# Optimization experiments

Hardware: AMD Instinct MI355X
Metric: run time of the kernel (lower is better)

The kernel has to match this reference:

```python
import math
import jax, jax.numpy as jnp
import numpy as np

N, D, E, H = 4096, 512, 64, 8
LN_EPS = 1e-5


def setup_inputs() -> dict:
    key = jax.random.key(0)
    ks = jax.random.split(key, 6)
    return {
        "x": jax.random.normal(ks[0], (N, D), jnp.float32),
        "wq": jax.random.normal(ks[1], (H, D, E), jnp.float32) * 0.05,
        "wk": jax.random.normal(ks[2], (H, D, E), jnp.float32) * 0.05,
        "wv": jax.random.normal(ks[3], (H, D, E), jnp.float32) * 0.05,
        "w_mh": jax.random.normal(ks[4], (H * E, D), jnp.float32) * 0.05,
        "ln1_g": jnp.ones((D,), jnp.float32),
        "ln1_b": jnp.zeros((D,), jnp.float32),
        "ffn_w": jax.random.normal(ks[5], (D, D), jnp.float32) * 0.05,  # torch Linear weight [out,in]
        "ffn_b": jnp.zeros((D,), jnp.float32),
        "ln2_g": jnp.ones((D,), jnp.float32),
        "ln2_b": jnp.zeros((D,), jnp.float32),
    }


def _layernorm(y, g, b):
    m = y.mean(-1, keepdims=True)
    v = ((y - m) ** 2).mean(-1, keepdims=True)
    return (y - m) * jax.lax.rsqrt(v + LN_EPS) * g + b


def reference(x, wq, wk, wv, w_mh, ln1_g, ln1_b, ffn_w, ffn_b, ln2_g, ln2_b):
    dk = math.sqrt(wk.shape[-1])  # sqrt(embedding_size), as in the torch code
    q = jnp.einsum('nd,hde->hne', x, wq)  # [H,N,E]
    k = jnp.einsum('nd,hde->hne', x, wk)
    v = jnp.einsum('nd,hde->hne', x, wv)
    scores = jax.nn.softmax(jnp.einsum('hne,hme->hnm', q, k) / dk, axis=-1)  # [H,N,N]
    z = jnp.einsum('hnm,hme->hne', scores, v)  # [H,N,E]
    concat_z = jnp.transpose(z, (1, 0, 2)).reshape(x.shape[0], -1)  # [N, H*E]
    transformed_z = concat_z @ w_mh  # [N, D]
    normed_z = _layernorm(transformed_z + x, ln1_g, ln1_b)
    out = normed_z @ ffn_w.T + ffn_b  # nn.Linear
    return _layernorm(out + normed_z, ln2_g, ln2_b)
```

## Files before the change

kernel.cpp:

```cpp
#include <hip/hip_runtime.h>

#define NN 4096
#define DD 512
#define EE 64
#define HH 8

typedef _Float16 f16;
typedef f16 f16x4 __attribute__((ext_vector_type(4)));
typedef f16 f16x8 __attribute__((ext_vector_type(8)));
typedef float f32x4 __attribute__((ext_vector_type(4)));

__global__ __launch_bounds__(256) void cvt_kernel(const float* __restrict__ s, f16* __restrict__ d, int n)
{
    int i = (blockIdx.x * 256 + threadIdx.x) * 4;
    if (i < n) {
        float4 t = *(const float4*)(s + i);
        f16x4 h = { (f16)t.x, (f16)t.y, (f16)t.z, (f16)t.w };
        *(f16x4*)(d + i) = h;
    }
}

__global__ __launch_bounds__(256) void transpose_cvt_kernel(
    const float* __restrict__ src, f16* __restrict__ dst, int R, int C)
{
    __shared__ float t[32][33];
    const int z = blockIdx.z;
    src += (size_t)z * R * C;
    dst += (size_t)z * R * C;
    const int bx = blockIdx.x * 32;
    const int by = blockIdx.y * 32;
    const int tx = threadIdx.x & 31;
    const int ty = threadIdx.x >> 5;
    #pragma unroll
    for (int i = 0; i < 4; ++i) {
        int r = ty + i * 8;
        t[r][tx] = src[(size_t)(by + r) * C + bx + tx];
    }
    __syncthreads();
    #pragma unroll
    for (int i = 0; i < 4; ++i) {
        int c = ty + i * 8;
        dst[(size_t)(bx + c) * R + by + tx] = (f16)t[tx][c];
    }
}

__global__ __launch_bounds__(256) void qkv_mfma_kernel(
    const f16* __restrict__ A, const f16* __restrict__ BT,
    f16* __restrict__ qh, f16* __restrict__ kh, f16* __restrict__ vTh)
{
    __shared__ f16 As[64][72];
    __shared__ f16 Bs[64][72];
    const int tid = threadIdx.x;
    const int n0 = blockIdx.x * 64;
    const int cb = blockIdx.y;
    const int sel = cb >> 3, h = cb & 7;
    const f16* Arow = A + (size_t)n0 * DD;
    const f16* Brow = BT + (size_t)cb * 64 * DD;

    const int lane = tid & 63, wave = tid >> 6;
    const int l16 = lane & 15, quad = lane >> 4;
    const int m0 = wave * 16;

    f32x4 acc[4];
    #pragma unroll
    for (int t = 0; t < 4; ++t) acc[t] = (f32x4){0.f, 0.f, 0.f, 0.f};

    for (int kt = 0; kt < DD; kt += 64) {
        __syncthreads();
        #pragma unroll
        for (int i = 0; i < 2; ++i) {
            int idx = tid + i * 256;
            int r = idx >> 3, c8 = (idx & 7) * 8;
            *(f16x8*)(&As[r][c8]) = *(const f16x8*)(Arow + (size_t)r * DD + kt + c8);
            *(f16x8*)(&Bs[r][c8]) = *(const f16x8*)(Brow + (size_t)r * DD + kt + c8);
        }
        __syncthreads();
        #pragma unroll
        for (int kk = 0; kk < 64; kk += 32) {
            f16x8 a = *(const f16x8*)(&As[m0 + l16][kk + quad * 8]);
            #pragma unroll
            for (int t = 0; t < 4; ++t) {
                f16x8 b = *(const f16x8*)(&Bs[t * 16 + l16][kk + quad * 8]);
                acc[t] = __builtin_amdgcn_mfma_f32_16x16x32_f16(a, b, acc[t], 0, 0, 0);
            }
        }
    }

    if (sel == 2) {
        #pragma unroll
        for (int t = 0; t < 4; ++t) {
            int e = t * 16 + l16;
            #pragma unroll
            for (int r = 0; r < 4; ++r)
                vTh[((size_t)h * EE + e) * NN + n0 + m0 + quad * 4 + r] = (f16)acc[t][r];
        }
    } else {
        f16* o = (sel == 0) ? qh : kh;
        const float s = (sel == 0) ? 0.125f : 1.0f;
        #pragma unroll
        for (int r = 0; r < 4; ++r) {
            int row = n0 + m0 + quad * 4 + r;
            #pragma unroll
            for (int t = 0; t < 4; ++t)
                o[(size_t)h * NN * EE + (size_t)row * EE + t * 16 + l16] = (f16)(acc[t][r] * s);
        }
    }
}

#define BQ 64
#define BK 64
#define SPLITS 2
#define LQ (EE + 8)
#define LV (BK + 12)

__global__ __launch_bounds__(256) void attn_mfma_kernel(
    const f16* __restrict__ q, const f16* __restrict__ k,
    const f16* __restrict__ vT, float* __restrict__ Opart, float* __restrict__ lpart)
{
    __shared__ f16 Qs[BQ][LQ];
    __shared__ f16 Ks[BK][LQ];
    __shared__ f16 VsT[EE][LV];
    __shared__ f16 Ps[BQ][LV];

    const int tid = threadIdx.x;
    const int h = blockIdx.y;
    const int n0 = blockIdx.x * BQ;
    const int sp = blockIdx.z;
    const int wave = tid >> 6;
    const int lane = tid & 63;
    const int l16 = lane & 15;
    const int quad = lane >> 4;
    const int m0 = wave * 16;

    const f16* qh = q + (size_t)h * NN * EE;
    const f16* kh = k + (size_t)h * NN * EE;
    const f16* vh = vT + (size_t)h * NN * EE;

    #pragma unroll
    for (int i = 0; i < 2; ++i) {
        int idx = tid + i * 256;
        int row = idx >> 3, c8 = (idx & 7) * 8;
        *(f16x8*)(&Qs[row][c8]) = *(const f16x8*)(qh + (size_t)(n0 + row) * EE + c8);
    }
    __syncthreads();

    f16x8 qf0 = *(const f16x8*)(&Qs[m0 + l16][quad * 8]);
    f16x8 qf1 = *(const f16x8*)(&Qs[m0 + l16][32 + quad * 8]);

    float lp[4] = {0.f, 0.f, 0.f, 0.f};
    f32x4 O[4];
    #pragma unroll
    for (int t = 0; t < 4; ++t) O[t] = (f32x4){0.f, 0.f, 0.f, 0.f};

    const int k_begin = sp * (NN / SPLITS);
    const int k_end = k_begin + (NN / SPLITS);

    const int srow = tid >> 3, sc8 = (tid & 7) * 8;
    const int srow2 = (tid + 256) >> 3, sc82 = ((tid + 256) & 7) * 8;

    f16x8 kr0 = *(const f16x8*)(kh + (size_t)(k_begin + srow) * EE + sc8);
    f16x8 kr1 = *(const f16x8*)(kh + (size_t)(k_begin + srow2) * EE + sc82);
    f16x8 vr0 = *(const f16x8*)(vh + (size_t)srow * NN + k_begin + sc8);
    f16x8 vr1 = *(const f16x8*)(vh + (size_t)srow2 * NN + k_begin + sc82);

    for (int kt = k_begin; kt < k_end; kt += BK) {
        __syncthreads();
        *(f16x8*)(&Ks[srow][sc8]) = kr0;
        *(f16x8*)(&Ks[srow2][sc82]) = kr1;
        *(f16x8*)(&VsT[srow][sc8]) = vr0;
        *(f16x8*)(&VsT[srow2][sc82]) = vr1;
        __syncthreads();

        if (kt + BK < k_end) {
            kr0 = *(const f16x8*)(kh + (size_t)(kt + BK + srow) * EE + sc8);
            kr1 = *(const f16x8*)(kh + (size_t)(kt + BK + srow2) * EE + sc82);
            vr0 = *(const f16x8*)(vh + (size_t)srow * NN + kt + BK + sc8);
            vr1 = *(const f16x8*)(vh + (size_t)srow2 * NN + kt + BK + sc82);
        }

        f32x4 S[4];
        #pragma unroll
        for (int t = 0; t < 4; ++t) {
            f16x8 b0 = *(const f16x8*)(&Ks[t * 16 + l16][quad * 8]);
            f16x8 b1 = *(const f16x8*)(&Ks[t * 16 + l16][32 + quad * 8]);
            f32x4 s = {0.f, 0.f, 0.f, 0.f};
            s = __builtin_amdgcn_mfma_f32_16x16x32_f16(qf0, b0, s, 0, 0, 0);
            s = __builtin_amdgcn_mfma_f32_16x16x32_f16(qf1, b1, s, 0, 0, 0);
            S[t] = s;
        }

        #pragma unroll
        for (int r = 0; r < 4; ++r) {
            float p0 = __expf(S[0][r]);
            float p1 = __expf(S[1][r]);
            float p2 = __expf(S[2][r]);
            float p3 = __expf(S[3][r]);
            lp[r] += (p0 + p1) + (p2 + p3);
            const int prow = m0 + quad * 4 + r;
            Ps[prow][0 * 16 + l16] = (f16)p0;
            Ps[prow][1 * 16 + l16] = (f16)p1;
            Ps[prow][2 * 16 + l16] = (f16)p2;
            Ps[prow][3 * 16 + l16] = (f16)p3;
        }

        f16x8 a0 = *(const f16x8*)(&Ps[m0 + l16][quad * 8]);
        f16x8 a1 = *(const f16x8*)(&Ps[m0 + l16][32 + quad * 8]);
        #pragma unroll
        for (int t = 0; t < 4; ++t) {
            f16x8 b0 = *(const f16x8*)(&VsT[t * 16 + l16][quad * 8]);
            f16x8 b1 = *(const f16x8*)(&VsT[t * 16 + l16][32 + quad * 8]);
            O[t] = __builtin_amdgcn_mfma_f32_16x16x32_f16(a0, b0, O[t], 0, 0, 0);
            O[t] = __builtin_amdgcn_mfma_f32_16x16x32_f16(a1, b1, O[t], 0, 0, 0);
        }
    }

    #pragma unroll
    for (int r = 0; r < 4; ++r) {
        float s = lp[r];
        s += __shfl_xor(s, 1);
        s += __shfl_xor(s, 2);
        s += __shfl_xor(s, 4);
        s += __shfl_xor(s, 8);
        const int row = n0 + m0 + quad * 4 + r;
        if (l16 == 0)
            lpart[(size_t)sp * HH * NN + (size_t)h * NN + row] = s;
        #pragma unroll
        for (int t = 0; t < 4; ++t)
            Opart[(size_t)sp * NN * DD + (size_t)row * DD + h * EE + t * 16 + l16] = O[t][r];
    }
}

__global__ __launch_bounds__(256) void attn_combine_kernel(
    const float* __restrict__ Opart, const float* __restrict__ lpart, f16* __restrict__ zh)
{
    const size_t idx = ((size_t)blockIdx.x * 256 + threadIdx.x) * 8;
    const int n = (int)(idx >> 9);
    const int c = (int)(idx & 511);
    const int h = c >> 6;
    const float l = lpart[(size_t)h * NN + n] + lpart[(size_t)HH * NN + (size_t)h * NN + n];
    const float inv = 1.f / l;
    f32x4 a0 = *(const f32x4*)(Opart + idx);
    f32x4 a1 = *(const f32x4*)(Opart + idx + 4);
    f32x4 b0 = *(const f32x4*)(Opart + (size_t)NN * DD + idx);
    f32x4 b1 = *(const f32x4*)(Opart + (size_t)NN * DD + idx + 4);
    f16x8 o;
    #pragma unroll
    for (int i = 0; i < 4; ++i) {
        o[i]     = (f16)((a0[i] + b0[i]) * inv);
        o[i + 4] = (f16)((a1[i] + b1[i]) * inv);
    }
    *(f16x8*)(zh + idx) = o;
}

__global__ __launch_bounds__(256) void gemm_mfma_kernel(
    const f16* __restrict__ A, const f16* __restrict__ BT,
    const float* __restrict__ bias, const float* __restrict__ resid32,
    const f16* __restrict__ resid16, float* __restrict__ out)
{
    __shared__ f16 As[64][72];
    __shared__ f16 Bs[64][72];
    const int tid = threadIdx.x;
    const int n0 = blockIdx.x * 64;
    const int j0 = blockIdx.y * 64;
    const f16* Arow = A + (size_t)n0 * DD;
    const f16* Brow = BT + (size_t)j0 * DD;

    const int lane = tid & 63, wave = tid >> 6;
    const int l16 = lane & 15, quad = lane >> 4;
    const int m0 = wave * 16;

    f32x4 acc[4];
    #pragma unroll
    for (int t = 0; t < 4; ++t) acc[t] = (f32x4){0.f, 0.f, 0.f, 0.f};

    for (int kt = 0; kt < DD; kt += 64) {
        __syncthreads();
        #pragma unroll
        for (int i = 0; i < 2; ++i) {
            int idx = tid + i * 256;
            int r = idx >> 3, c8 = (idx & 7) * 8;
            *(f16x8*)(&As[r][c8]) = *(const f16x8*)(Arow + (size_t)r * DD + kt + c8);
            *(f16x8*)(&Bs[r][c8]) = *(const f16x8*)(Brow + (size_t)r * DD + kt + c8);
        }
        __syncthreads();
        #pragma unroll
        for (int kk = 0; kk < 64; kk += 32) {
            f16x8 a = *(const f16x8*)(&As[m0 + l16][kk + quad * 8]);
            #pragma unroll
            for (int t = 0; t < 4; ++t) {
                f16x8 b = *(const f16x8*)(&Bs[t * 16 + l16][kk + quad * 8]);
                acc[t] = __builtin_amdgcn_mfma_f32_16x16x32_f16(a, b, acc[t], 0, 0, 0);
            }
        }
    }

    #pragma unroll
    for (int r = 0; r < 4; ++r) {
        int row = n0 + m0 + quad * 4 + r;
        #pragma unroll
        for (int t = 0; t < 4; ++t) {
            int col = j0 + t * 16 + l16;
            float v = acc[t][r];
            if (bias)    v += bias[col];
            if (resid32) v += resid32[(size_t)row * DD + col];
            if (resid16) v += (float)resid16[(size_t)row * DD + col];
            out[(size_t)row * DD + col] = v;
        }
    }
}

__global__ __launch_bounds__(256) void ln_kernel(
    const float* __restrict__ y, const float* __restrict__ g, const float* __restrict__ b,
    f16* __restrict__ oh, float* __restrict__ of)
{
    const int lane = threadIdx.x & 63, wave = threadIdx.x >> 6;
    const int row = blockIdx.x * 4 + wave;
    const float* yr = y + (size_t)row * DD;
    f32x4 v0 = *(const f32x4*)(yr + lane * 4);
    f32x4 v1 = *(const f32x4*)(yr + 256 + lane * 4);
    float s = (v0[0] + v0[1]) + (v0[2] + v0[3]) + (v1[0] + v1[1]) + (v1[2] + v1[3]);
    float q = (v0[0]*v0[0] + v0[1]*v0[1]) + (v0[2]*v0[2] + v0[3]*v0[3])
            + (v1[0]*v1[0] + v1[1]*v1[1]) + (v1[2]*v1[2] + v1[3]*v1[3]);
    #pragma unroll
    for (int o = 1; o < 64; o <<= 1) { s += __shfl_xor(s, o); q += __shfl_xor(q, o); }
    float mean = s * (1.f / DD);
    float var = q * (1.f / DD) - mean * mean;
    float inv = rsqrtf(var + 1e-5f);

    f32x4 g0 = *(const f32x4*)(g + lane * 4);
    f32x4 g1 = *(const f32x4*)(g + 256 + lane * 4);
    f32x4 b0 = *(const f32x4*)(b + lane * 4);
    f32x4 b1 = *(const f32x4*)(b + 256 + lane * 4);
    f32x4 o0, o1;
    #pragma unroll
    for (int i = 0; i < 4; ++i) {
        o0[i] = (v0[i] - mean) * inv * g0[i] + b0[i];
        o1[i] = (v1[i] - mean) * inv * g1[i] + b1[i];
    }
    if (oh) {
        f16x4 h0 = { (f16)o0[0], (f16)o0[1], (f16)o0[2], (f16)o0[3] };
        f16x4 h1 = { (f16)o1[0], (f16)o1[1], (f16)o1[2], (f16)o1[3] };
        *(f16x4*)(oh + (size_t)row * DD + lane * 4) = h0;
        *(f16x4*)(oh + (size_t)row * DD + 256 + lane * 4) = h1;
    }
    if (of) {
        *(f32x4*)(of + (size_t)row * DD + lane * 4) = o0;
        *(f32x4*)(of + (size_t)row * DD + 256 + lane * 4) = o1;
    }
}

extern "C" void kernel_launch(void* const* d_in, const int* in_sizes, int n_in,
                              void* d_out, int out_size, void* d_ws, size_t ws_size,
                              hipStream_t stream) {
    const float* x     = (const float*)d_in[0];
    const float* wq    = (const float*)d_in[1];
    const float* wk    = (const float*)d_in[2];
    const float* wv    = (const float*)d_in[3];
    const float* w_mh  = (const float*)d_in[4];
    const float* ln1_g = (const float*)d_in[5];
    const float* ln1_b = (const float*)d_in[6];
    const float* ffn_w = (const float*)d_in[7];
    const float* ffn_b = (const float*)d_in[8];
    const float* ln2_g = (const float*)d_in[9];
    const float* ln2_b = (const float*)d_in[10];
    float* out = (float*)d_out;

    char* base = (char*)d_ws;
    float* Opart = (float*)base;
    float* lpart = Opart + (size_t)2 * NN * DD;
    f16* xh   = (f16*)base;
    float* y  = (float*)base;
    f16* p = (f16*)(base + ((size_t)2 * NN * DD + (size_t)2 * HH * NN) * sizeof(float));
    f16* wqkvT  = p; p += (size_t)3 * HH * EE * DD;
    f16* wmhT   = p; p += (size_t)DD * DD;
    f16* ffnT   = p; p += (size_t)DD * DD;
    f16* qh     = p; p += (size_t)HH * NN * EE;
    f16* kh     = p; p += (size_t)HH * NN * EE;
    f16* vTh    = p; p += (size_t)HH * NN * EE;
    f16* zh     = p; p += (size_t)NN * DD;
    f16* nzh    = p; p += (size_t)NN * DD;

    cvt_kernel<<<dim3(NN * DD / 1024), 256, 0, stream>>>(x, xh, NN * DD);
    cvt_kernel<<<dim3(DD * DD / 1024), 256, 0, stream>>>(ffn_w, ffnT, DD * DD);
    transpose_cvt_kernel<<<dim3(EE / 32, DD / 32, HH), 256, 0, stream>>>(wq, wqkvT, DD, EE);
    transpose_cvt_kernel<<<dim3(EE / 32, DD / 32, HH), 256, 0, stream>>>(wk, wqkvT + (size_t)HH * EE * DD, DD, EE);
    transpose_cvt_kernel<<<dim3(EE / 32, DD / 32, HH), 256, 0, stream>>>(wv, wqkvT + (size_t)2 * HH * EE * DD, DD, EE);
    transpose_cvt_kernel<<<dim3(DD / 32, DD / 32, 1), 256, 0, stream>>>(w_mh, wmhT, DD, DD);

    qkv_mfma_kernel<<<dim3(NN / 64, 24), 256, 0, stream>>>(xh, wqkvT, qh, kh, vTh);
    attn_mfma_kernel<<<dim3(NN / BQ, HH, SPLITS), 256, 0, stream>>>(qh, kh, vTh, Opart, lpart);
    attn_combine_kernel<<<dim3(NN * DD / 2048), 256, 0, stream>>>(Opart, lpart, zh);
    gemm_mfma_kernel<<<dim3(NN / 64, DD / 64), 256, 0, stream>>>(zh, wmhT, nullptr, x, nullptr, y);
    ln_kernel<<<dim3(NN / 4), 256, 0, stream>>>(y, ln1_g, ln1_b, nzh, nullptr);
    gemm_mfma_kernel<<<dim3(NN / 64, DD / 64), 256, 0, stream>>>(nzh, ffnT, ffn_b, nullptr, nzh, y);
    ln_kernel<<<dim3(NN / 4), 256, 0, stream>>>(y, ln2_g, ln2_b, nullptr, out);
}
```

Before: 217.1 us.

## Compute transposed attention scores so P stays in registers, use exp2, adaptive splits

```diff
diff --git a/kernel.cpp b/kernel.cpp
--- a/kernel.cpp
+++ b/kernel.cpp
@@ -9,6 +9,8 @@
 typedef f16 f16x4 __attribute__((ext_vector_type(4)));
 typedef f16 f16x8 __attribute__((ext_vector_type(8)));
 typedef float f32x4 __attribute__((ext_vector_type(4)));
+
+__device__ __forceinline__ float hexp2(float x) { return __builtin_amdgcn_exp2f(x); }
 
 __global__ __launch_bounds__(256) void cvt_kernel(const float* __restrict__ s, f16* __restrict__ d, int n)
 {
@@ -96,7 +98,7 @@
         }
     } else {
         f16* o = (sel == 0) ? qh : kh;
-        const float s = (sel == 0) ? 0.125f : 1.0f;
+        const float s = (sel == 0) ? 0.125f * 1.44269504088896f : 1.0f;
         #pragma unroll
         for (int r = 0; r < 4; ++r) {
             int row = n0 + m0 + quad * 4 + r;
@@ -109,23 +111,20 @@
 
 #define BQ 64
 #define BK 64
-#define SPLITS 2
-#define LQ (EE + 8)
-#define LV (BK + 12)
+#define LK (BK + 12)
 
 __global__ __launch_bounds__(256) void attn_mfma_kernel(
     const f16* __restrict__ q, const f16* __restrict__ k,
     const f16* __restrict__ vT, float* __restrict__ Opart, float* __restrict__ lpart)
 {
-    __shared__ f16 Qs[BQ][LQ];
-    __shared__ f16 Ks[BK][LQ];
-    __shared__ f16 VsT[EE][LV];
-    __shared__ f16 Ps[BQ][LV];
+    __shared__ f16 Ks[BK][LK];
+    __shared__ f16 VsT[EE][LK];
 
     const int tid = threadIdx.x;
     const int h = blockIdx.y;
     const int n0 = blockIdx.x * BQ;
     const int sp = blockIdx.z;
+    const int nsp = gridDim.z;
     const int wave = tid >> 6;
     const int lane = tid & 63;
     const int l16 = lane & 15;
@@ -136,27 +135,22 @@
     const f16* kh = k + (size_t)h * NN * EE;
     const f16* vh = vT + (size_t)h * NN * EE;
 
-    #pragma unroll
-    for (int i = 0; i < 2; ++i) {
-        int idx = tid + i * 256;
-        int row = idx >> 3, c8 = (idx & 7) * 8;
-        *(f16x8*)(&Qs[row][c8]) = *(const f16x8*)(qh + (size_t)(n0 + row) * EE + c8);
-    }
-    __syncthreads();
-
-    f16x8 qf0 = *(const f16x8*)(&Qs[m0 + l16][quad * 8]);
-    f16x8 qf1 = *(const f16x8*)(&Qs[m0 + l16][32 + quad * 8]);
-
-    float lp[4] = {0.f, 0.f, 0.f, 0.f};
+    f16x8 qf0 = *(const f16x8*)(qh + (size_t)(n0 + m0 + l16) * EE + quad * 8);
+    f16x8 qf1 = *(const f16x8*)(qh + (size_t)(n0 + m0 + l16) * EE + 32 + quad * 8);
+
+    float lp = 0.f;
     f32x4 O[4];
     #pragma unroll
     for (int t = 0; t < 4; ++t) O[t] = (f32x4){0.f, 0.f, 0.f, 0.f};
 
-    const int k_begin = sp * (NN / SPLITS);
-    const int k_end = k_begin + (NN / SPLITS);
+    const int span = NN / nsp;
+    const int k_begin = sp * span;
+    const int k_end = k_begin + span;
 
     const int srow = tid >> 3, sc8 = (tid & 7) * 8;
     const int srow2 = (tid + 256) >> 3, sc82 = ((tid + 256) & 7) * 8;
+    #define KPERM(kk_) (((kk_) & 0x23) | (((kk_) & 0x04) << 2) | (((kk_) & 0x18) >> 1))
+    const int prow1 = KPERM(srow), prow2 = KPERM(srow2);
 
     f16x8 kr0 = *(const f16x8*)(kh + (size_t)(k_begin + srow) * EE + sc8);
     f16x8 kr1 = *(const f16x8*)(kh + (size_t)(k_begin + srow2) * EE + sc82);
@@ -165,8 +159,8 @@
 
     for (int kt = k_begin; kt < k_end; kt += BK) {
         __syncthreads();
-        *(f16x8*)(&Ks[srow][sc8]) = kr0;
-        *(f16x8*)(&Ks[srow2][sc82]) = kr1;
+        *(f16x8*)(&Ks[prow1][sc8]) = kr0;
+        *(f16x8*)(&Ks[prow2][sc82]) = kr1;
         *(f16x8*)(&VsT[srow][sc8]) = vr0;
         *(f16x8*)(&VsT[srow2][sc82]) = vr1;
         __syncthreads();
@@ -178,76 +172,69 @@
             vr1 = *(const f16x8*)(vh + (size_t)srow2 * NN + kt + BK + sc82);
         }
 
-        f32x4 S[4];
+        f32x4 st[4];
         #pragma unroll
         for (int t = 0; t < 4; ++t) {
-            f16x8 b0 = *(const f16x8*)(&Ks[t * 16 + l16][quad * 8]);
-            f16x8 b1 = *(const f16x8*)(&Ks[t * 16 + l16][32 + quad * 8]);
+            f16x8 a0 = *(const f16x8*)(&Ks[t * 16 + l16][quad * 8]);
+            f16x8 a1 = *(const f16x8*)(&Ks[t * 16 + l16][32 + quad * 8]);
             f32x4 s = {0.f, 0.f, 0.f, 0.f};
-            s = __builtin_amdgcn_mfma_f32_16x16x32_f16(qf0, b0, s, 0, 0, 0);
-            s = __builtin_amdgcn_mfma_f32_16x16x32_f16(qf1, b1, s, 0, 0, 0);
-            S[t] = s;
-        }
-
-        #pragma unroll
-        for (int r = 0; r < 4; ++r) {
-            float p0 = __expf(S[0][r]);
-            float p1 = __expf(S[1][r]);
-            float p2 = __expf(S[2][r]);
-            float p3 = __expf(S[3][r]);
-            lp[r] += (p0 + p1) + (p2 + p3);
-            const int prow = m0 + quad * 4 + r;
-            Ps[prow][0 * 16 + l16] = (f16)p0;
-            Ps[prow][1 * 16 + l16] = (f16)p1;
-            Ps[prow][2 * 16 + l16] = (f16)p2;
-            Ps[prow][3 * 16 + l16] = (f16)p3;
-        }
-
-        f16x8 a0 = *(const f16x8*)(&Ps[m0 + l16][quad * 8]);
-        f16x8 a1 = *(const f16x8*)(&Ps[m0 + l16][32 + quad * 8]);
+            s = __builtin_amdgcn_mfma_f32_16x16x32_f16(a0, qf0, s, 0, 0, 0);
+            s = __builtin_amdgcn_mfma_f32_16x16x32_f16(a1, qf1, s, 0, 0, 0);
+            st[t] = s;
+        }
+
+        f16x8 bf[2];
         #pragma unroll
         for (int t = 0; t < 4; ++t) {
-            f16x8 b0 = *(const f16x8*)(&VsT[t * 16 + l16][quad * 8]);
-            f16x8 b1 = *(const f16x8*)(&VsT[t * 16 + l16][32 + quad * 8]);
-            O[t] = __builtin_amdgcn_mfma_f32_16x16x32_f16(a0, b0, O[t], 0, 0, 0);
-            O[t] = __builtin_amdgcn_mfma_f32_16x16x32_f16(a1, b1, O[t], 0, 0, 0);
-        }
-    }
-
-    #pragma unroll
-    for (int r = 0; r < 4; ++r) {
-        float s = lp[r];
-        s += __shfl_xor(s, 1);
-        s += __shfl_xor(s, 2);
-        s += __shfl_xor(s, 4);
-        s += __shfl_xor(s, 8);
-        const int row = n0 + m0 + quad * 4 + r;
-        if (l16 == 0)
-            lpart[(size_t)sp * HH * NN + (size_t)h * NN + row] = s;
-        #pragma unroll
-        for (int t = 0; t < 4; ++t)
-            Opart[(size_t)sp * NN * DD + (size_t)row * DD + h * EE + t * 16 + l16] = O[t][r];
-    }
+            float p0 = hexp2(st[t][0]);
+            float p1 = hexp2(st[t][1]);
+            float p2 = hexp2(st[t][2]);
+            float p3 = hexp2(st[t][3]);
+            lp += (p0 + p1) + (p2 + p3);
+            f16x8& b = bf[t >> 1];
+            const int o = (t & 1) * 4;
+            b[o + 0] = (f16)p0; b[o + 1] = (f16)p1;
+            b[o + 2] = (f16)p2; b[o + 3] = (f16)p3;
+        }
+
+        #pragma unroll
+        for (int te = 0; te < 4; ++te) {
+            f16x8 v0 = *(const f16x8*)(&VsT[te * 16 + l16][quad * 8]);
+            f16x8 v1 = *(const f16x8*)(&VsT[te * 16 + l16][32 + quad * 8]);
+            O[te] = __builtin_amdgcn_mfma_f32_16x16x32_f16(v0, bf[0], O[te], 0, 0, 0);
+            O[te] = __builtin_amdgcn_mfma_f32_16x16x32_f16(v1, bf[1], O[te], 0, 0, 0);
+        }
+    }
+
+    const int row = n0 + m0 + l16;
+    lp += __shfl_xor(lp, 16);
+    lp += __shfl_xor(lp, 32);
+    if (quad == 0)
+        lpart[(size_t)sp * HH * NN + (size_t)h * NN + row] = lp;
+    #pragma unroll
+    for (int te = 0; te < 4; ++te)
+        *(f32x4*)(Opart + ((size_t)sp * NN + row) * DD + h * EE + te * 16 + quad * 4) = O[te];
 }
 
 __global__ __launch_bounds__(256) void attn_combine_kernel(
-    const float* __restrict__ Opart, const float* __restrict__ lpart, f16* __restrict__ zh)
+    const float* __restrict__ Opart, const float* __restrict__ lpart, f16* __restrict__ zh, int nsp)
 {
     const size_t idx = ((size_t)blockIdx.x * 256 + threadIdx.x) * 8;
     const int n = (int)(idx >> 9);
-    const int c = (int)(idx & 511);
-    const int h = c >> 6;
-    const float l = lpart[(size_t)h * NN + n] + lpart[(size_t)HH * NN + (size_t)h * NN + n];
+    const int h = (int)((idx & 511) >> 6);
+    float l = 0.f;
+    for (int s = 0; s < nsp; ++s) l += lpart[(size_t)s * HH * NN + (size_t)h * NN + n];
     const float inv = 1.f / l;
-    f32x4 a0 = *(const f32x4*)(Opart + idx);
-    f32x4 a1 = *(const f32x4*)(Opart + idx + 4);
-    f32x4 b0 = *(const f32x4*)(Opart + (size_t)NN * DD + idx);
-    f32x4 b1 = *(const f32x4*)(Opart + (size_t)NN * DD + idx + 4);
+    f32x4 a0 = {0.f,0.f,0.f,0.f}, a1 = {0.f,0.f,0.f,0.f};
+    for (int s = 0; s < nsp; ++s) {
+        a0 += *(const f32x4*)(Opart + (size_t)s * NN * DD + idx);
+        a1 += *(const f32x4*)(Opart + (size_t)s * NN * DD + idx + 4);
+    }
     f16x8 o;
     #pragma unroll
     for (int i = 0; i < 4; ++i) {
-        o[i]     = (f16)((a0[i] + b0[i]) * inv);
-        o[i + 4] = (f16)((a1[i] + b1[i]) * inv);
+        o[i]     = (f16)(a0[i] * inv);
+        o[i + 4] = (f16)(a1[i] * inv);
     }
     *(f16x8*)(zh + idx) = o;
 }
@@ -365,12 +352,23 @@
     const float* ln2_b = (const float*)d_in[10];
     float* out = (float*)d_out;
 
+    const size_t poolHalfs = (size_t)3 * HH * EE * DD + 2 * (size_t)DD * DD
+                           + 3 * (size_t)HH * NN * EE + 2 * (size_t)NN * DD;
+    int SP = 2;
+    {
+        size_t need4 = ((size_t)4 * NN * DD + 4 * HH * NN) * 4 + poolHalfs * 2 + 1024;
+        size_t need3 = ((size_t)3 * NN * DD + 3 * HH * NN) * 4 + poolHalfs * 2 + 1024;
+        if (ws_size >= need4) SP = 4; else if (ws_size >= need3) SP = 3;
+    }
+
     char* base = (char*)d_ws;
     float* Opart = (float*)base;
-    float* lpart = Opart + (size_t)2 * NN * DD;
+    float* lpart = Opart + (size_t)SP * NN * DD;
     f16* xh   = (f16*)base;
     float* y  = (float*)base;
-    f16* p = (f16*)(base + ((size_t)2 * NN * DD + (size_t)2 * HH * NN) * sizeof(float));
+    size_t regionA = ((size_t)SP * NN * DD + (size_t)SP * HH * NN) * sizeof(float);
+    regionA = (regionA + 255) & ~(size_t)255;
+    f16* p = (f16*)(base + regionA);
     f16* wqkvT  = p; p += (size_t)3 * HH * EE * DD;
     f16* wmhT   = p; p += (size_t)DD * DD;
     f16* ffnT   = p; p += (size_t)DD * DD;
@@ -388,8 +386,8 @@
     transpose_cvt_kernel<<<dim3(DD / 32, DD / 32, 1), 256, 0, stream>>>(w_mh, wmhT, DD, DD);
 
     qkv_mfma_kernel<<<dim3(NN / 64, 24), 256, 0, stream>>>(xh, wqkvT, qh, kh, vTh);
-    attn_mfma_kernel<<<dim3(NN / BQ, HH, SPLITS), 256, 0, stream>>>(qh, kh, vTh, Opart, lpart);
-    attn_combine_kernel<<<dim3(NN * DD / 2048), 256, 0, stream>>>(Opart, lpart, zh);
+    attn_mfma_kernel<<<dim3(NN / BQ, HH, SP), 256, 0, stream>>>(qh, kh, vTh, Opart, lpart);
+    attn_combine_kernel<<<dim3(NN * DD / 2048), 256, 0, stream>>>(Opart, lpart, zh, SP);
     gemm_mfma_kernel<<<dim3(NN / 64, DD / 64), 256, 0, stream>>>(zh, wmhT, nullptr, x, nullptr, y);
     ln_kernel<<<dim3(NN / 4), 256, 0, stream>>>(y, ln1_g, ln1_b, nzh, nullptr);
     gemm_mfma_kernel<<<dim3(NN / 64, DD / 64), 256, 0, stream>>>(nzh, ffnT, ffn_b, nullptr, nzh, y);
```

Measured after the change: 201.8 us. 1.08x faster.
